# Kernel optimization log

Measured on AMD Instinct MI355X. Metric: run time of the kernel, lower is better.

The kernel has to match this reference:

```python
import jax, jax.numpy as jnp
import numpy as np

L, B, S, H = 13, 32, 128, 768   # encoder hidden states: layers, batch (hardcoded 32), seq, hidden
U = 32                          # num_gru_units
G = 2 * U                       # linear out dim / bidirectional GRU feature dim (64)
NL = 2                          # num_labels
EPS = 1e-3                      # keras LayerNormalization default epsilon


def setup_inputs() -> dict:
    key = jax.random.key(0)
    ks = jax.random.split(key, 10)
    def n(k, shape, scale=0.05):
        return (jax.random.normal(k, shape, jnp.float32) * scale).astype(jnp.float32)
    return {
        "xs": jax.random.normal(ks[0], (L, B, S, H), jnp.float32),
        "W_lin": n(ks[1], (H, G)),
        "b_lin": jnp.zeros((G,), jnp.float32),
        "ln_gamma": jnp.ones((G,), jnp.float32),
        "ln_beta": jnp.zeros((G,), jnp.float32),
        "Wk_f": n(ks[2], (G, 3 * U)),
        "Wr_f": n(ks[3], (U, 3 * U)),
        "b_f": jnp.zeros((2, 3 * U), jnp.float32),   # [input_bias, recurrent_bias] (reset_after=True)
        "Wk_b": n(ks[4], (G, 3 * U)),
        "Wr_b": n(ks[5], (U, 3 * U)),
        "b_b": jnp.zeros((2, 3 * U), jnp.float32),
        "W_cls": n(ks[6], (G, NL)),
        "b_cls": jnp.zeros((NL,), jnp.float32),
    }


def _layernorm(x, g, b):
    m = jnp.mean(x, axis=-1, keepdims=True)
    v = jnp.var(x, axis=-1, keepdims=True)
    return (x - m) * jax.lax.rsqrt(v + EPS) * g + b


def _gru_dir(seq, h0, Wk, Wr, bias):
    # Keras GRU v2 cell (reset_after=True). seq: [B,S,G], h0: [B,U]
    xp = jnp.einsum('bsg,gk->bsk', seq, Wk) + bias[0]  # [B,S,3U]
    def step(h, x_t):
        rec = h @ Wr + bias[1]                          # [B,3U]
        z = jax.nn.sigmoid(x_t[:, :U] + rec[:, :U])
        r = jax.nn.sigmoid(x_t[:, U:2 * U] + rec[:, U:2 * U])
        hh = jnp.tanh(x_t[:, 2 * U:] + r * rec[:, 2 * U:])
        hn = z * h + (1.0 - z) * hh
        return hn, hn
    hT, ys = jax.lax.scan(step, h0, jnp.swapaxes(xp, 0, 1))  # scan over time
    return jnp.swapaxes(ys, 0, 1), hT                        # [B,S,U], [B,U]


def reference(xs, W_lin, b_lin, ln_gamma, ln_beta,
              Wk_f, Wr_f, b_f, Wk_b, Wr_b, b_b, W_cls, b_cls):
    # _forward: loop over the 13 encoder hidden-state layers; the bidirectional
    # GRU output feeds back as a residual into the next layer's linear output.
    # Dropout layers are treated as identity (deterministic reference), under
    # which the 100-pass MC average equals a single pass.
    seq = jnp.zeros((B, S, G), xs.dtype)  # initial 'sequence' of zeros
    h1 = jnp.zeros((B, U), xs.dtype)      # initial_state=None -> zeros in keras
    h2 = jnp.zeros((B, U), xs.dtype)
    for i in range(L):
        x = _layernorm(xs[i] @ W_lin + b_lin + seq, ln_gamma, ln_beta)  # [B,S,G]
        out_f, h1 = _gru_dir(x, h1, Wk_f, Wr_f, b_f)
        out_b, h2 = _gru_dir(x[:, ::-1], h2, Wk_b, Wr_b, b_b)
        seq = jnp.concatenate([out_f, out_b[:, ::-1]], axis=-1)         # [B,S,2U]
    # tf.stack([h1,h2], -1) -> [B,U,2]; reshape [32,-1] interleaves fwd/bwd units
    hcat = jnp.stack([h1, h2], axis=-1).reshape(B, -1)                  # [B,2U]
    return jax.nn.softmax(hcat @ W_cls + b_cls, axis=-1)                # [B,NL]
```

## Files before the change

kernel.cpp:

```cpp
#include <hip/hip_runtime.h>
#include <hip/hip_fp16.h>

#define L_ 13
#define B_ 32
#define S_ 128
#define H_ 768
#define NU 32
#define GG 64
#define TU 96
#define LN_EPS 1e-3f
#define SEQ_ST 68
#define XT_ST 129
#define WK_ST 100
#define XPH_ST 100

#define DPP_X1  0xB1
#define DPP_X2  0x4E
#define DPP_X7  0x141
#define DPP_X15 0x140

typedef float v2f __attribute__((ext_vector_type(2)));
typedef _Float16 h2t __attribute__((ext_vector_type(2)));
typedef unsigned int uv2 __attribute__((ext_vector_type(2)));

union F4H8 { float4 f4; __half2 hh[4]; h2t h[4]; };
union FH2  { float f; __half2 hh; h2t h; };
union F2H2 { float2 f2; __half2 hh[2]; };

__device__ __forceinline__ float sigmoidf_(float a) { return 1.0f / (1.0f + __expf(-a)); }
__device__ __forceinline__ float tanhf_(float a) { float e = __expf(-2.0f * a); return (1.0f - e) / (1.0f + e); }
__device__ __forceinline__ void pkfma(v2f& a, v2f x, v2f w) {
    asm("v_pk_fma_f32 %0, %1, %2, %0" : "+v"(a) : "v"(x), "v"(w));
}
template <int CTRL>
__device__ __forceinline__ float dppf(float x) {
    return __int_as_float(__builtin_amdgcn_update_dpp(
        0, __float_as_int(x), CTRL, 0xF, 0xF, true));
}
__device__ __forceinline__ float pairsum16(float x) {
#if __has_builtin(__builtin_amdgcn_permlane16_swap)
    uv2 s = __builtin_amdgcn_permlane16_swap(
        __float_as_uint(x), __float_as_uint(x), false, false);
    return __uint_as_float(s.x) + __uint_as_float(s.y);
#else
    return x + __shfl_xor(x, 16);
#endif
}

__global__ __launch_bounds__(256) void lin_kernel(
    const float* __restrict__ xs, const float* __restrict__ Wl,
    const float* __restrict__ bl, __half* __restrict__ lin)
{
    __shared__ float sA[64][68];
    __shared__ float sW[64][68];
    const int t = threadIdx.x;
    const size_t row0 = (size_t)blockIdx.x * 64;
    const int r4 = (t >> 4) << 2;
    const int c4 = (t & 15) << 2;

    float acc[4][4];
    #pragma unroll
    for (int i = 0; i < 4; ++i)
        #pragma unroll
        for (int j = 0; j < 4; ++j) acc[i][j] = 0.f;

    for (int kt = 0; kt < H_; kt += 64) {
        #pragma unroll
        for (int p = 0; p < 4; ++p) {
            int idx = t + 256 * p;
            int r = idx >> 4, cc = (idx & 15) << 2;
            *(float4*)&sA[r][cc] = *(const float4*)&xs[(row0 + r) * H_ + kt + cc];
            *(float4*)&sW[r][cc] = *(const float4*)&Wl[(size_t)(kt + r) * GG + cc];
        }
        __syncthreads();
        #pragma unroll 8
        for (int k = 0; k < 64; ++k) {
            float a0 = sA[r4 + 0][k], a1 = sA[r4 + 1][k], a2 = sA[r4 + 2][k], a3 = sA[r4 + 3][k];
            float4 w = *(const float4*)&sW[k][c4];
            acc[0][0] += a0 * w.x; acc[0][1] += a0 * w.y; acc[0][2] += a0 * w.z; acc[0][3] += a0 * w.w;
            acc[1][0] += a1 * w.x; acc[1][1] += a1 * w.y; acc[1][2] += a1 * w.z; acc[1][3] += a1 * w.w;
            acc[2][0] += a2 * w.x; acc[2][1] += a2 * w.y; acc[2][2] += a2 * w.z; acc[2][3] += a2 * w.w;
            acc[3][0] += a3 * w.x; acc[3][1] += a3 * w.y; acc[3][2] += a3 * w.z; acc[3][3] += a3 * w.w;
        }
        __syncthreads();
    }
    float4 bv = *(const float4*)&bl[c4];
    #pragma unroll
    for (int i = 0; i < 4; ++i) {
        F2H2 u;
        u.hh[0] = __floats2half2_rn(acc[i][0] + bv.x, acc[i][1] + bv.y);
        u.hh[1] = __floats2half2_rn(acc[i][2] + bv.z, acc[i][3] + bv.w);
        *(float2*)&lin[(row0 + r4 + i) * GG + c4] = u.f2;
    }
}

__global__ __launch_bounds__(512) void chain_kernel(
    const __half* __restrict__ lin_all,
    const float* __restrict__ Wr_f, const float* __restrict__ b_f,
    const float* __restrict__ Wr_b, const float* __restrict__ b_b,
    const float* __restrict__ Wk_f, const float* __restrict__ Wk_b,
    const float* __restrict__ ln_g, const float* __restrict__ ln_b,
    const float* __restrict__ W_cls, const float* __restrict__ b_cls,
    float* __restrict__ out)
{
    extern __shared__ float sm[];
    float*   seqb = sm;
    __half2* xt2  = (__half2*)(sm + 8704);
    __half2* wk2  = (__half2*)(sm + 8704 + 4128);
    __half*  xph  = (__half*)(sm + 8704 + 4128 + 6400);
    float*   hbf  = sm + 8704 + 4128 + 6400 + 12800;
    float*   hbb  = hbf + NU;

    const int b = blockIdx.x;
    const int t = threadIdx.x;
    const int wave = t >> 6;
    const int lane = t & 63;
    const int v16 = lane & 15;
    const int b4 = (lane >> 4) & 1;
    const int b5 = (lane >> 5) & 1;
    const int ud = v16 + 16 * b5;

    for (int i = t; i < S_ * SEQ_ST; i += 512) seqb[i] = 0.f;
    for (int i = t; i < 2 * 32 * 96; i += 512) {
        const int d = i / 3072, rem = i - d * 3072, k2 = rem / 96, c = rem - k2 * 96;
        const float* W = d ? Wk_b : Wk_f;
        wk2[(d * 32 + k2) * WK_ST + c] =
            __floats2half2_rn(W[(2 * k2) * TU + c], W[(2 * k2 + 1) * TU + c]);
    }

    v2f wz[8], wr_[8], wh[8];
    float h_store = 0.f, h_dot = 0.f, rbz2 = 0.f, rbr2 = 0.f, rbh2 = 0.f;
    if (wave < 2) {
        const float* Wr   = wave ? Wr_b : Wr_f;
        const float* bias = wave ? b_b  : b_f;
        const int ex[8] = {0, 2, 7, 5, 15, 13, 8, 10};
        const int ey[8] = {1, 3, 6, 4, 14, 12, 9, 11};
        const int BB = 16 * b4;
        #pragma unroll
        for (int m = 0; m < 8; ++m) {
            const int jx = BB + (v16 ^ ex[m]), jy = BB + (v16 ^ ey[m]);
            wz[m]  = v2f{ Wr[jx * TU + ud],          Wr[jy * TU + ud] };
            wr_[m] = v2f{ Wr[jx * TU + NU + ud],     Wr[jy * TU + NU + ud] };
            wh[m]  = v2f{ Wr[jx * TU + 2 * NU + ud], Wr[jy * TU + 2 * NU + ud] };
        }
        rbz2 = 0.5f * bias[TU + ud];
        rbr2 = 0.5f * bias[TU + NU + ud];
        rbh2 = 0.5f * bias[TU + 2 * NU + ud];
    }

    const int g8 = t >> 3;
    const int c8 = (t & 7) << 3;
    const int rgrp = t & 31;
    const int cg = t >> 5;
    const int dsel = cg >> 3;
    const int cc = (cg & 7) * 12;
    const float* bias0 = dsel ? b_b : b_f;
    const __half2* wkd = wk2 + dsel * 32 * WK_ST;
    __half* xpd = xph + dsel * (S_ * XPH_ST);

    __syncthreads();

    for (int l = 0; l < L_; ++l) {
        const __half* linb = lin_all + (size_t)(l * B_ + b) * S_ * GG;

        #pragma unroll
        for (int p = 0; p < 2; ++p) {
            const int r = g8 + 64 * p;
            F4H8 lu; lu.f4 = *(const float4*)&linb[(size_t)r * GG + c8];
            float4 s0 = *(const float4*)&seqb[r * SEQ_ST + c8];
            float4 s1 = *(const float4*)&seqb[r * SEQ_ST + c8 + 4];
            float2 l0 = __half22float2(lu.hh[0]);
            float2 l1 = __half22float2(lu.hh[1]);
            float2 l2 = __half22float2(lu.hh[2]);
            float2 l3 = __half22float2(lu.hh[3]);
            float v[8];
            v[0] = l0.x + s0.x; v[1] = l0.y + s0.y; v[2] = l1.x + s0.z; v[3] = l1.y + s0.w;
            v[4] = l2.x + s1.x; v[5] = l2.y + s1.y; v[6] = l3.x + s1.z; v[7] = l3.y + s1.w;
            float s = 0.f;
            #pragma unroll
            for (int j = 0; j < 8; ++j) s += v[j];
            #pragma unroll
            for (int off = 1; off < 8; off <<= 1) s += __shfl_xor(s, off);
            const float mean = s * 0.015625f;
            float q = 0.f;
            float d[8];
            #pragma unroll
            for (int j = 0; j < 8; ++j) { d[j] = v[j] - mean; q += d[j] * d[j]; }
            #pragma unroll
            for (int off = 1; off < 8; off <<= 1) q += __shfl_xor(q, off);
            const float rstd = rsqrtf(q * 0.015625f + LN_EPS);
            float4 g0 = *(const float4*)&ln_g[c8];
            float4 g1 = *(const float4*)&ln_g[c8 + 4];
            float4 b0 = *(const float4*)&ln_b[c8];
            float4 b1 = *(const float4*)&ln_b[c8 + 4];
            float x[8];
            x[0] = d[0] * rstd * g0.x + b0.x; x[1] = d[1] * rstd * g0.y + b0.y;
            x[2] = d[2] * rstd * g0.z + b0.z; x[3] = d[3] * rstd * g0.w + b0.w;
            x[4] = d[4] * rstd * g1.x + b1.x; x[5] = d[5] * rstd * g1.y + b1.y;
            x[6] = d[6] * rstd * g1.z + b1.z; x[7] = d[7] * rstd * g1.w + b1.w;
            #pragma unroll
            for (int j = 0; j < 4; ++j)
                xt2[(c8 / 2 + j) * XT_ST + r] = __floats2half2_rn(x[2 * j], x[2 * j + 1]);
        }
        __syncthreads();

        {
            float acc[4][12];
            #pragma unroll
            for (int m = 0; m < 12; ++m) {
                const float bi = bias0[cc + m];
                acc[0][m] = bi; acc[1][m] = bi; acc[2][m] = bi; acc[3][m] = bi;
            }
            #pragma unroll 4
            for (int k2 = 0; k2 < 32; ++k2) {
                FH2 x0, x1, x2, x3;
                x0.hh = xt2[k2 * XT_ST + rgrp];
                x1.hh = xt2[k2 * XT_ST + rgrp + 32];
                x2.hh = xt2[k2 * XT_ST + rgrp + 64];
                x3.hh = xt2[k2 * XT_ST + rgrp + 96];
                F4H8 wa, wb, wc;
                wa.f4 = *(const float4*)&wkd[k2 * WK_ST + cc];
                wb.f4 = *(const float4*)&wkd[k2 * WK_ST + cc + 4];
                wc.f4 = *(const float4*)&wkd[k2 * WK_ST + cc + 8];
                #pragma unroll
                for (int m = 0; m < 4; ++m) {
                    acc[0][m]     = __builtin_amdgcn_fdot2(x0.h, wa.h[m], acc[0][m],     false);
                    acc[1][m]     = __builtin_amdgcn_fdot2(x1.h, wa.h[m], acc[1][m],     false);
                    acc[2][m]     = __builtin_amdgcn_fdot2(x2.h, wa.h[m], acc[2][m],     false);
                    acc[3][m]     = __builtin_amdgcn_fdot2(x3.h, wa.h[m], acc[3][m],     false);
                    acc[0][m + 4] = __builtin_amdgcn_fdot2(x0.h, wb.h[m], acc[0][m + 4], false);
                    acc[1][m + 4] = __builtin_amdgcn_fdot2(x1.h, wb.h[m], acc[1][m + 4], false);
                    acc[2][m + 4] = __builtin_amdgcn_fdot2(x2.h, wb.h[m], acc[2][m + 4], false);
                    acc[3][m + 4] = __builtin_amdgcn_fdot2(x3.h, wb.h[m], acc[3][m + 4], false);
                    acc[0][m + 8] = __builtin_amdgcn_fdot2(x0.h, wc.h[m], acc[0][m + 8], false);
                    acc[1][m + 8] = __builtin_amdgcn_fdot2(x1.h, wc.h[m], acc[1][m + 8], false);
                    acc[2][m + 8] = __builtin_amdgcn_fdot2(x2.h, wc.h[m], acc[2][m + 8], false);
                    acc[3][m + 8] = __builtin_amdgcn_fdot2(x3.h, wc.h[m], acc[3][m + 8], false);
                }
            }
            #pragma unroll
            for (int i = 0; i < 4; ++i) {
                const int r = rgrp + 32 * i;
                __half2* dst = (__half2*)&xpd[r * XPH_ST + cc];
                #pragma unroll
                for (int j = 0; j < 6; ++j)
                    dst[j] = __floats2half2_rn(acc[i][2 * j], acc[i][2 * j + 1]);
            }
        }
        __syncthreads();

        if (wave < 2) {
            const int dir = wave;
            const __half* xp = xph + dir * (S_ * XPH_ST);
            float* sq = seqb + dir * NU + (lane & 31);
            const int stp = dir ? -1 : 1;
            int s = dir ? (S_ - 1) : 0;
            const bool wl = (lane < 32);
            const bool fix = (b4 != b5);
            float xz = (float)xp[s * XPH_ST + ud];
            float xr = (float)xp[s * XPH_ST + 32 + ud];
            float xh = (float)xp[s * XPH_ST + 64 + ud];
            for (int st = 0; st < S_; ++st) {
                float nz = 0.f, nr = 0.f, nh = 0.f;
                if (st < S_ - 1) {
                    const int sn = s + stp;
                    nz = (float)xp[sn * XPH_ST + ud];
                    nr = (float)xp[sn * XPH_ST + 32 + ud];
                    nh = (float)xp[sn * XPH_ST + 64 + ud];
                }
                v2f ro[8];
                ro[0].x = h_store;                ro[0].y = dppf<DPP_X1>(h_store);
                ro[1].x = dppf<DPP_X2>(ro[0].x);  ro[1].y = dppf<DPP_X2>(ro[0].y);
                ro[2].x = dppf<DPP_X7>(ro[0].x);  ro[2].y = dppf<DPP_X7>(ro[0].y);
                ro[3].x = dppf<DPP_X7>(ro[1].x);  ro[3].y = dppf<DPP_X7>(ro[1].y);
                ro[4].x = dppf<DPP_X15>(ro[0].x); ro[4].y = dppf<DPP_X15>(ro[0].y);
                ro[5].x = dppf<DPP_X15>(ro[1].x); ro[5].y = dppf<DPP_X15>(ro[1].y);
                ro[6].x = dppf<DPP_X15>(ro[2].x); ro[6].y = dppf<DPP_X15>(ro[2].y);
                ro[7].x = dppf<DPP_X15>(ro[3].x); ro[7].y = dppf<DPP_X15>(ro[3].y);

                v2f az = v2f{0.5f * xz + rbz2, 0.f};
                v2f ar = v2f{0.5f * xr + rbr2, 0.f};
                v2f ah = v2f{rbh2, 0.f};
                #pragma unroll
                for (int m = 0; m < 8; ++m) {
                    pkfma(az, ro[m], wz[m]);
                    pkfma(ar, ro[m], wr_[m]);
                    pkfma(ah, ro[m], wh[m]);
                }
                const float pz = pairsum16(az.x + az.y);
                const float pr = pairsum16(ar.x + ar.y);
                const float ph = pairsum16(ah.x + ah.y);

                const float z  = sigmoidf_(pz);
                const float r  = sigmoidf_(pr);
                const float hh = tanhf_(xh + r * ph);
                const float hn_raw = hh + z * (h_dot - hh);
                h_dot = hn_raw;
                uv2 s32 = __builtin_amdgcn_permlane32_swap(
                    __float_as_uint(hn_raw), __float_as_uint(hn_raw), false, false);
                const float v32 = wl ? __uint_as_float(s32.y) : __uint_as_float(s32.x);
                h_store = fix ? v32 : hn_raw;
                if (wl) sq[s * SEQ_ST] = h_store;
                s += stp; xz = nz; xr = nr; xh = nh;
            }
        }
        __syncthreads();
    }

    if (wave < 2 && lane < 32) (wave ? hbb : hbf)[lane & 31] = h_store;
    __syncthreads();
    if (t == 0) {
        float l0 = b_cls[0], l1 = b_cls[1];
        for (int j = 0; j < NU; ++j) {
            const float hf = hbf[j], hk = hbb[j];
            l0 += hf * W_cls[4 * j]     + hk * W_cls[4 * j + 2];
            l1 += hf * W_cls[4 * j + 1] + hk * W_cls[4 * j + 3];
        }
        const float m = fmaxf(l0, l1);
        const float e0 = __expf(l0 - m), e1 = __expf(l1 - m);
        const float inv = 1.0f / (e0 + e1);
        out[b * 2 + 0] = e0 * inv;
        out[b * 2 + 1] = e1 * inv;
    }
}

extern "C" void kernel_launch(void* const* d_in, const int* in_sizes, int n_in,
                              void* d_out, int out_size, void* d_ws, size_t ws_size,
                              hipStream_t stream) {
    const float* xs    = (const float*)d_in[0];
    const float* W_lin = (const float*)d_in[1];
    const float* b_lin = (const float*)d_in[2];
    const float* ln_g  = (const float*)d_in[3];
    const float* ln_b  = (const float*)d_in[4];
    const float* Wk_f  = (const float*)d_in[5];
    const float* Wr_f  = (const float*)d_in[6];
    const float* b_f   = (const float*)d_in[7];
    const float* Wk_b  = (const float*)d_in[8];
    const float* Wr_b  = (const float*)d_in[9];
    const float* b_b   = (const float*)d_in[10];
    const float* W_cls = (const float*)d_in[11];
    const float* b_cls = (const float*)d_in[12];
    float* out = (float*)d_out;

    __half* lin_all = (__half*)d_ws;

    const int smem = (8704 + 4128 + 6400 + 12800 + 64) * (int)sizeof(float);
    (void)hipFuncSetAttribute((const void*)chain_kernel,
                              hipFuncAttributeMaxDynamicSharedMemorySize, smem);

    lin_kernel<<<(L_ * B_ * S_) / 64, 256, 0, stream>>>(xs, W_lin, b_lin, lin_all);

    chain_kernel<<<B_, 512, smem, stream>>>(
        lin_all, Wr_f, b_f, Wr_b, b_b, Wk_f, Wk_b, ln_g, ln_b, W_cls, b_cls, out);
}
```

Measured before the change: 639.8 us.

## Overlap per-layer LayerNorm and input projection with GRU recurrence via LDS flags

Replaces the block-wide barrier sequence (LN, projection GEMM, recurrence) with producer/consumer specialization inside the block. Six waves compute LN and the input projection in row chunks ordered from the sequence centre outward. They publish completion counters in LDS, and the two recurrence waves poll those counters before consuming each chunk. The recurrence waves likewise publish progress so the next layer's chunks can start as soon as their inputs are ready. Separately, the activations now use exp2 and rcp with log2e prescaling folded into the weights and biases, and the accumulation chains are split in two to shorten dependencies. The spin-waits with sleep add polling overhead and carry some ordering risk.

```diff
diff --git a/kernel.cpp b/kernel.cpp
--- a/kernel.cpp
+++ b/kernel.cpp
@@ -10,15 +10,23 @@
 #define TU 96
 #define LN_EPS 1e-3f
 #define SEQ_ST 68
-#define XT_ST 129
 #define WK_ST 100
 #define XPH_ST 100
+#define K1f 1.4426950408889634f
+#define K2f 2.8853900817779268f
 
 #define DPP_X1  0xB1
 #define DPP_X2  0x4E
 #define DPP_X7  0x141
 #define DPP_X15 0x140
 
+#define OFF_WK   8704
+#define OFF_XPH  (OFF_WK + 6400)
+#define OFF_XT2  (OFF_XPH + 12800)
+#define OFF_HB   (OFF_XT2 + 3456)
+#define OFF_FLG  (OFF_HB + 64)
+#define SMEM_FLOATS (OFF_FLG + 32)
+
 typedef float v2f __attribute__((ext_vector_type(2)));
 typedef _Float16 h2t __attribute__((ext_vector_type(2)));
 typedef unsigned int uv2 __attribute__((ext_vector_type(2)));
@@ -27,8 +35,6 @@
 union FH2  { float f; __half2 hh; h2t h; };
 union F2H2 { float2 f2; __half2 hh[2]; };
 
-__device__ __forceinline__ float sigmoidf_(float a) { return 1.0f / (1.0f + __expf(-a)); }
-__device__ __forceinline__ float tanhf_(float a) { float e = __expf(-2.0f * a); return (1.0f - e) / (1.0f + e); }
 __device__ __forceinline__ void pkfma(v2f& a, v2f x, v2f w) {
     asm("v_pk_fma_f32 %0, %1, %2, %0" : "+v"(a) : "v"(x), "v"(w));
 }
@@ -45,6 +51,16 @@
 #else
     return x + __shfl_xor(x, 16);
 #endif
+}
+__device__ __forceinline__ int chunk_of(int r) {
+    return (r < 64) ? ((63 - r) >> 3) : ((r - 64) >> 3);
+}
+__device__ __forceinline__ void poll_ge(unsigned* p, unsigned tgt) {
+    int gd = 0;
+    while (__hip_atomic_load(p, __ATOMIC_ACQUIRE, __HIP_MEMORY_SCOPE_WORKGROUP) < tgt) {
+        __builtin_amdgcn_s_sleep(1);
+        if (++gd > (1 << 24)) break;
+    }
 }
 
 __global__ __launch_bounds__(256) void lin_kernel(
@@ -104,12 +120,14 @@
     float* __restrict__ out)
 {
     extern __shared__ float sm[];
-    float*   seqb = sm;
-    __half2* xt2  = (__half2*)(sm + 8704);
-    __half2* wk2  = (__half2*)(sm + 8704 + 4128);
-    __half*  xph  = (__half*)(sm + 8704 + 4128 + 6400);
-    float*   hbf  = sm + 8704 + 4128 + 6400 + 12800;
-    float*   hbb  = hbf + NU;
+    float*    seqb   = sm;
+    __half2*  wk2    = (__half2*)(sm + OFF_WK);
+    __half*   xph    = (__half*)(sm + OFF_XPH);
+    __half2*  xt2all = (__half2*)(sm + OFF_XT2);
+    float*    hbf    = sm + OFF_HB;
+    float*    hbb    = hbf + NU;
+    unsigned* seq_blk = (unsigned*)(sm + OFF_FLG);
+    unsigned* gemcnt  = seq_blk + 16;
 
     const int b = blockIdx.x;
     const int t = threadIdx.x;
@@ -121,11 +139,13 @@
     const int ud = v16 + 16 * b5;
 
     for (int i = t; i < S_ * SEQ_ST; i += 512) seqb[i] = 0.f;
+    if (t < 24) seq_blk[t] = 0u;
     for (int i = t; i < 2 * 32 * 96; i += 512) {
         const int d = i / 3072, rem = i - d * 3072, k2 = rem / 96, c = rem - k2 * 96;
         const float* W = d ? Wk_b : Wk_f;
+        const float sc = (c >= 64) ? K2f : K1f;
         wk2[(d * 32 + k2) * WK_ST + c] =
-            __floats2half2_rn(W[(2 * k2) * TU + c], W[(2 * k2 + 1) * TU + c]);
+            __floats2half2_rn(W[(2 * k2) * TU + c] * sc, W[(2 * k2 + 1) * TU + c] * sc);
     }
 
     v2f wz[8], wr_[8], wh[8];
@@ -139,134 +159,45 @@
         #pragma unroll
         for (int m = 0; m < 8; ++m) {
             const int jx = BB + (v16 ^ ex[m]), jy = BB + (v16 ^ ey[m]);
-            wz[m]  = v2f{ Wr[jx * TU + ud],          Wr[jy * TU + ud] };
-            wr_[m] = v2f{ Wr[jx * TU + NU + ud],     Wr[jy * TU + NU + ud] };
-            wh[m]  = v2f{ Wr[jx * TU + 2 * NU + ud], Wr[jy * TU + 2 * NU + ud] };
-        }
-        rbz2 = 0.5f * bias[TU + ud];
-        rbr2 = 0.5f * bias[TU + NU + ud];
-        rbh2 = 0.5f * bias[TU + 2 * NU + ud];
-    }
-
-    const int g8 = t >> 3;
-    const int c8 = (t & 7) << 3;
-    const int rgrp = t & 31;
-    const int cg = t >> 5;
-    const int dsel = cg >> 3;
-    const int cc = (cg & 7) * 12;
-    const float* bias0 = dsel ? b_b : b_f;
-    const __half2* wkd = wk2 + dsel * 32 * WK_ST;
-    __half* xpd = xph + dsel * (S_ * XPH_ST);
+            wz[m]  = v2f{ K1f * Wr[jx * TU + ud],          K1f * Wr[jy * TU + ud] };
+            wr_[m] = v2f{ K1f * Wr[jx * TU + NU + ud],     K1f * Wr[jy * TU + NU + ud] };
+            wh[m]  = v2f{ K2f * Wr[jx * TU + 2 * NU + ud], K2f * Wr[jy * TU + 2 * NU + ud] };
+        }
+        rbz2 = 0.5f * K1f * bias[TU + ud];
+        rbr2 = 0.5f * K1f * bias[TU + NU + ud];
+        rbh2 = 0.5f * K2f * bias[TU + 2 * NU + ud];
+    }
 
     __syncthreads();
 
-    for (int l = 0; l < L_; ++l) {
-        const __half* linb = lin_all + (size_t)(l * B_ + b) * S_ * GG;
-
-        #pragma unroll
-        for (int p = 0; p < 2; ++p) {
-            const int r = g8 + 64 * p;
-            F4H8 lu; lu.f4 = *(const float4*)&linb[(size_t)r * GG + c8];
-            float4 s0 = *(const float4*)&seqb[r * SEQ_ST + c8];
-            float4 s1 = *(const float4*)&seqb[r * SEQ_ST + c8 + 4];
-            float2 l0 = __half22float2(lu.hh[0]);
-            float2 l1 = __half22float2(lu.hh[1]);
-            float2 l2 = __half22float2(lu.hh[2]);
-            float2 l3 = __half22float2(lu.hh[3]);
-            float v[8];
-            v[0] = l0.x + s0.x; v[1] = l0.y + s0.y; v[2] = l1.x + s0.z; v[3] = l1.y + s0.w;
-            v[4] = l2.x + s1.x; v[5] = l2.y + s1.y; v[6] = l3.x + s1.z; v[7] = l3.y + s1.w;
-            float s = 0.f;
-            #pragma unroll
-            for (int j = 0; j < 8; ++j) s += v[j];
-            #pragma unroll
-            for (int off = 1; off < 8; off <<= 1) s += __shfl_xor(s, off);
-            const float mean = s * 0.015625f;
-            float q = 0.f;
-            float d[8];
-            #pragma unroll
-            for (int j = 0; j < 8; ++j) { d[j] = v[j] - mean; q += d[j] * d[j]; }
-            #pragma unroll
-            for (int off = 1; off < 8; off <<= 1) q += __shfl_xor(q, off);
-            const float rstd = rsqrtf(q * 0.015625f + LN_EPS);
-            float4 g0 = *(const float4*)&ln_g[c8];
-            float4 g1 = *(const float4*)&ln_g[c8 + 4];
-            float4 b0 = *(const float4*)&ln_b[c8];
-            float4 b1 = *(const float4*)&ln_b[c8 + 4];
-            float x[8];
-            x[0] = d[0] * rstd * g0.x + b0.x; x[1] = d[1] * rstd * g0.y + b0.y;
-            x[2] = d[2] * rstd * g0.z + b0.z; x[3] = d[3] * rstd * g0.w + b0.w;
-            x[4] = d[4] * rstd * g1.x + b1.x; x[5] = d[5] * rstd * g1.y + b1.y;
-            x[6] = d[6] * rstd * g1.z + b1.z; x[7] = d[7] * rstd * g1.w + b1.w;
-            #pragma unroll
-            for (int j = 0; j < 4; ++j)
-                xt2[(c8 / 2 + j) * XT_ST + r] = __floats2half2_rn(x[2 * j], x[2 * j + 1]);
-        }
-        __syncthreads();
-
-        {
-            float acc[4][12];
-            #pragma unroll
-            for (int m = 0; m < 12; ++m) {
-                const float bi = bias0[cc + m];
-                acc[0][m] = bi; acc[1][m] = bi; acc[2][m] = bi; acc[3][m] = bi;
-            }
-            #pragma unroll 4
-            for (int k2 = 0; k2 < 32; ++k2) {
-                FH2 x0, x1, x2, x3;
-                x0.hh = xt2[k2 * XT_ST + rgrp];
-                x1.hh = xt2[k2 * XT_ST + rgrp + 32];
-                x2.hh = xt2[k2 * XT_ST + rgrp + 64];
-                x3.hh = xt2[k2 * XT_ST + rgrp + 96];
-                F4H8 wa, wb, wc;
-                wa.f4 = *(const float4*)&wkd[k2 * WK_ST + cc];
-                wb.f4 = *(const float4*)&wkd[k2 * WK_ST + cc + 4];
-                wc.f4 = *(const float4*)&wkd[k2 * WK_ST + cc + 8];
-                #pragma unroll
-                for (int m = 0; m < 4; ++m) {
-                    acc[0][m]     = __builtin_amdgcn_fdot2(x0.h, wa.h[m], acc[0][m],     false);
-                    acc[1][m]     = __builtin_amdgcn_fdot2(x1.h, wa.h[m], acc[1][m],     false);
-                    acc[2][m]     = __builtin_amdgcn_fdot2(x2.h, wa.h[m], acc[2][m],     false);
-                    acc[3][m]     = __builtin_amdgcn_fdot2(x3.h, wa.h[m], acc[3][m],     false);
-                    acc[0][m + 4] = __builtin_amdgcn_fdot2(x0.h, wb.h[m], acc[0][m + 4], false);
-                    acc[1][m + 4] = __builtin_amdgcn_fdot2(x1.h, wb.h[m], acc[1][m + 4], false);
-                    acc[2][m + 4] = __builtin_amdgcn_fdot2(x2.h, wb.h[m], acc[2][m + 4], false);
-                    acc[3][m + 4] = __builtin_amdgcn_fdot2(x3.h, wb.h[m], acc[3][m + 4], false);
-                    acc[0][m + 8] = __builtin_amdgcn_fdot2(x0.h, wc.h[m], acc[0][m + 8], false);
-                    acc[1][m + 8] = __builtin_amdgcn_fdot2(x1.h, wc.h[m], acc[1][m + 8], false);
-                    acc[2][m + 8] = __builtin_amdgcn_fdot2(x2.h, wc.h[m], acc[2][m + 8], false);
-                    acc[3][m + 8] = __builtin_amdgcn_fdot2(x3.h, wc.h[m], acc[3][m + 8], false);
-                }
-            }
-            #pragma unroll
-            for (int i = 0; i < 4; ++i) {
-                const int r = rgrp + 32 * i;
-                __half2* dst = (__half2*)&xpd[r * XPH_ST + cc];
-                #pragma unroll
-                for (int j = 0; j < 6; ++j)
-                    dst[j] = __floats2half2_rn(acc[i][2 * j], acc[i][2 * j + 1]);
-            }
-        }
-        __syncthreads();
-
-        if (wave < 2) {
-            const int dir = wave;
-            const __half* xp = xph + dir * (S_ * XPH_ST);
-            float* sq = seqb + dir * NU + (lane & 31);
-            const int stp = dir ? -1 : 1;
+    if (wave < 2) {
+        const int dir = wave;
+        const __half* xp = xph + dir * (S_ * XPH_ST);
+        float* sq = seqb + dir * NU + (lane & 31);
+        const int stp = dir ? -1 : 1;
+        const bool wl = (lane < 32);
+        const bool fix = (b4 != b5);
+
+        for (int L = 0; L < L_; ++L) {
+            unsigned dmask = 0;
+            poll_ge(&gemcnt[7], (unsigned)(L + 1));
+            dmask |= 1u << 7;
             int s = dir ? (S_ - 1) : 0;
-            const bool wl = (lane < 32);
-            const bool fix = (b4 != b5);
             float xz = (float)xp[s * XPH_ST + ud];
             float xr = (float)xp[s * XPH_ST + 32 + ud];
             float xh = (float)xp[s * XPH_ST + 64 + ud];
             for (int st = 0; st < S_; ++st) {
                 float nz = 0.f, nr = 0.f, nh = 0.f;
                 if (st < S_ - 1) {
-                    const int sn = s + stp;
-                    nz = (float)xp[sn * XPH_ST + ud];
-                    nr = (float)xp[sn * XPH_ST + 32 + ud];
-                    nh = (float)xp[sn * XPH_ST + 64 + ud];
+                    const int rp = s + stp;
+                    const int g = chunk_of(rp);
+                    if (!((dmask >> g) & 1u)) {
+                        poll_ge(&gemcnt[g], (unsigned)(L + 1));
+                        dmask |= 1u << g;
+                    }
+                    nz = (float)xp[rp * XPH_ST + ud];
+                    nr = (float)xp[rp * XPH_ST + 32 + ud];
+                    nh = (float)xp[rp * XPH_ST + 64 + ud];
                 }
                 v2f ro[8];
                 ro[0].x = h_store;                ro[0].y = dppf<DPP_X1>(h_store);
@@ -278,22 +209,25 @@
                 ro[6].x = dppf<DPP_X15>(ro[2].x); ro[6].y = dppf<DPP_X15>(ro[2].y);
                 ro[7].x = dppf<DPP_X15>(ro[3].x); ro[7].y = dppf<DPP_X15>(ro[3].y);
 
-                v2f az = v2f{0.5f * xz + rbz2, 0.f};
-                v2f ar = v2f{0.5f * xr + rbr2, 0.f};
-                v2f ah = v2f{rbh2, 0.f};
+                v2f aza = v2f{0.5f * xz + rbz2, 0.f}, azb = v2f{0.f, 0.f};
+                v2f ara = v2f{0.5f * xr + rbr2, 0.f}, arb = v2f{0.f, 0.f};
+                v2f aha = v2f{rbh2, 0.f},             ahb = v2f{0.f, 0.f};
                 #pragma unroll
-                for (int m = 0; m < 8; ++m) {
-                    pkfma(az, ro[m], wz[m]);
-                    pkfma(ar, ro[m], wr_[m]);
-                    pkfma(ah, ro[m], wh[m]);
-                }
-                const float pz = pairsum16(az.x + az.y);
-                const float pr = pairsum16(ar.x + ar.y);
-                const float ph = pairsum16(ah.x + ah.y);
-
-                const float z  = sigmoidf_(pz);
-                const float r  = sigmoidf_(pr);
-                const float hh = tanhf_(xh + r * ph);
+                for (int m = 0; m < 4; ++m) {
+                    pkfma(aza, ro[m], wz[m]);      pkfma(azb, ro[m + 4], wz[m + 4]);
+                    pkfma(ara, ro[m], wr_[m]);     pkfma(arb, ro[m + 4], wr_[m + 4]);
+                    pkfma(aha, ro[m], wh[m]);      pkfma(ahb, ro[m + 4], wh[m + 4]);
+                }
+                v2f azs = aza + azb, ars = ara + arb, ahs = aha + ahb;
+                const float pz = pairsum16(azs.x + azs.y);
+                const float pr = pairsum16(ars.x + ars.y);
+                const float ph = pairsum16(ahs.x + ahs.y);
+
+                const float z  = __builtin_amdgcn_rcpf(1.0f + __builtin_amdgcn_exp2f(-pz));
+                const float r  = __builtin_amdgcn_rcpf(1.0f + __builtin_amdgcn_exp2f(-pr));
+                const float tt = xh + r * ph;
+                const float et = __builtin_amdgcn_exp2f(-tt);
+                const float hh = (1.0f - et) * __builtin_amdgcn_rcpf(1.0f + et);
                 const float hn_raw = hh + z * (h_dot - hh);
                 h_dot = hn_raw;
                 uv2 s32 = __builtin_amdgcn_permlane32_swap(
@@ -301,13 +235,120 @@
                 const float v32 = wl ? __uint_as_float(s32.y) : __uint_as_float(s32.x);
                 h_store = fix ? v32 : hn_raw;
                 if (wl) sq[s * SEQ_ST] = h_store;
+                const bool pub = dir ? ((s & 15) == 0) : ((s & 15) == 15);
+                if (pub && lane == 0)
+                    __hip_atomic_store(&seq_blk[dir * 8 + (s >> 4)], (unsigned)(L + 1),
+                                       __ATOMIC_RELEASE, __HIP_MEMORY_SCOPE_WORKGROUP);
                 s += stp; xz = nz; xr = nr; xh = nh;
             }
         }
-        __syncthreads();
-    }
-
-    if (wave < 2 && lane < 32) (wave ? hbb : hbf)[lane & 31] = h_store;
+        if (wl) (dir ? hbb : hbf)[lane & 31] = h_store;
+    } else {
+        const int w = wave - 2;
+        __half2* xt2w = xt2all + w * 576;
+        const int c4 = (lane & 15) << 2;
+        const int g16 = lane >> 4;
+        const int lr4 = lane & 3;
+        const int cg = lane >> 2;
+        const int dsel = cg >> 3;
+        const int cc = (cg & 7) * 12;
+        const float* bias0 = dsel ? b_b : b_f;
+        const __half2* wkd = wk2 + dsel * 32 * WK_ST;
+        __half* xpd = xph + dsel * (S_ * XPH_ST);
+        float bsc[12];
+        #pragma unroll
+        for (int m = 0; m < 12; ++m)
+            bsc[m] = bias0[cc + m] * ((cc + m >= 64) ? K2f : K1f);
+
+        for (int L = 0; L < L_; ++L) {
+            const __half* linb = lin_all + (size_t)(L * B_ + b) * S_ * GG;
+            #pragma unroll 1
+            for (int g = 0; g < 8; ++g) {
+                if ((L * 8 + g) % 6 != w) continue;
+                const int bl = (56 - 8 * g) >> 4;
+                const int rA = 56 - 8 * g, rB = 64 + 8 * g;
+                poll_ge(&seq_blk[bl], (unsigned)L);
+                poll_ge(&seq_blk[7 - bl], (unsigned)L);
+                poll_ge(&seq_blk[8 + bl], (unsigned)L);
+                poll_ge(&seq_blk[8 + 7 - bl], (unsigned)L);
+
+                #pragma unroll
+                for (int p = 0; p < 4; ++p) {
+                    const int lr = 4 * p + g16;
+                    const int r = (lr < 8) ? (rA + lr) : (rB + lr - 8);
+                    F2H2 lu; lu.f2 = *(const float2*)&linb[(size_t)r * GG + c4];
+                    float4 sv = *(const float4*)&seqb[r * SEQ_ST + c4];
+                    float2 l0 = __half22float2(lu.hh[0]);
+                    float2 l1 = __half22float2(lu.hh[1]);
+                    float v0 = l0.x + sv.x, v1 = l0.y + sv.y, v2 = l1.x + sv.z, v3 = l1.y + sv.w;
+                    float s = v0 + v1 + v2 + v3;
+                    #pragma unroll
+                    for (int off = 1; off < 16; off <<= 1) s += __shfl_xor(s, off);
+                    const float mean = s * 0.015625f;
+                    const float d0 = v0 - mean, d1 = v1 - mean, d2 = v2 - mean, d3 = v3 - mean;
+                    float q = d0 * d0 + d1 * d1 + d2 * d2 + d3 * d3;
+                    #pragma unroll
+                    for (int off = 1; off < 16; off <<= 1) q += __shfl_xor(q, off);
+                    const float rstd = rsqrtf(q * 0.015625f + LN_EPS);
+                    float4 gm = *(const float4*)&ln_g[c4];
+                    float4 bt = *(const float4*)&ln_b[c4];
+                    const float x0 = d0 * rstd * gm.x + bt.x;
+                    const float x1 = d1 * rstd * gm.y + bt.y;
+                    const float x2 = d2 * rstd * gm.z + bt.z;
+                    const float x3 = d3 * rstd * gm.w + bt.w;
+                    const int k2a = (lane & 15) << 1;
+                    xt2w[(k2a + 0) * 18 + lr] = __floats2half2_rn(x0, x1);
+                    xt2w[(k2a + 1) * 18 + lr] = __floats2half2_rn(x2, x3);
+                }
+
+                float acc[4][12];
+                #pragma unroll
+                for (int m = 0; m < 12; ++m) {
+                    acc[0][m] = bsc[m]; acc[1][m] = bsc[m]; acc[2][m] = bsc[m]; acc[3][m] = bsc[m];
+                }
+                #pragma unroll 4
+                for (int k2 = 0; k2 < 32; ++k2) {
+                    FH2 x0, x1, x2, x3;
+                    x0.hh = xt2w[k2 * 18 + lr4];
+                    x1.hh = xt2w[k2 * 18 + lr4 + 4];
+                    x2.hh = xt2w[k2 * 18 + lr4 + 8];
+                    x3.hh = xt2w[k2 * 18 + lr4 + 12];
+                    F4H8 wa, wb, wc;
+                    wa.f4 = *(const float4*)&wkd[k2 * WK_ST + cc];
+                    wb.f4 = *(const float4*)&wkd[k2 * WK_ST + cc + 4];
+                    wc.f4 = *(const float4*)&wkd[k2 * WK_ST + cc + 8];
+                    #pragma unroll
+                    for (int m = 0; m < 4; ++m) {
+                        acc[0][m]     = __builtin_amdgcn_fdot2(x0.h, wa.h[m], acc[0][m],     false);
+                        acc[1][m]     = __builtin_amdgcn_fdot2(x1.h, wa.h[m], acc[1][m],     false);
+                        acc[2][m]     = __builtin_amdgcn_fdot2(x2.h, wa.h[m], acc[2][m],     false);
+                        acc[3][m]     = __builtin_amdgcn_fdot2(x3.h, wa.h[m], acc[3][m],     false);
+                        acc[0][m + 4] = __builtin_amdgcn_fdot2(x0.h, wb.h[m], acc[0][m + 4], false);
+                        acc[1][m + 4] = __builtin_amdgcn_fdot2(x1.h, wb.h[m], acc[1][m + 4], false);
+                        acc[2][m + 4] = __builtin_amdgcn_fdot2(x2.h, wb.h[m], acc[2][m + 4], false);
+                        acc[3][m + 4] = __builtin_amdgcn_fdot2(x3.h, wb.h[m], acc[3][m + 4], false);
+                        acc[0][m + 8] = __builtin_amdgcn_fdot2(x0.h, wc.h[m], acc[0][m + 8], false);
+                        acc[1][m + 8] = __builtin_amdgcn_fdot2(x1.h, wc.h[m], acc[1][m + 8], false);
+                        acc[2][m + 8] = __builtin_amdgcn_fdot2(x2.h, wc.h[m], acc[2][m + 8], false);
+                        acc[3][m + 8] = __builtin_amdgcn_fdot2(x3.h, wc.h[m], acc[3][m + 8], false);
+                    }
+                }
+                #pragma unroll
+                for (int i = 0; i < 4; ++i) {
+                    const int lr = lr4 + 4 * i;
+                    const int r = (lr < 8) ? (rA + lr) : (rB + lr - 8);
+                    __half2* dst = (__half2*)&xpd[r * XPH_ST + cc];
+                    #pragma unroll
+                    for (int j = 0; j < 6; ++j)
+                        dst[j] = __floats2half2_rn(acc[i][2 * j], acc[i][2 * j + 1]);
+                }
+                if (lane == 0)
+                    __hip_atomic_store(&gemcnt[g], (unsigned)(L + 1),
+                                       __ATOMIC_RELEASE, __HIP_MEMORY_SCOPE_WORKGROUP);
+            }
+        }
+    }
+
     __syncthreads();
     if (t == 0) {
         float l0 = b_cls[0], l1 = b_cls[1];
@@ -344,7 +385,7 @@
 
     __half* lin_all = (__half*)d_ws;
 
-    const int smem = (8704 + 4128 + 6400 + 12800 + 64) * (int)sizeof(float);
+    const int smem = SMEM_FLOATS * (int)sizeof(float);
     (void)hipFuncSetAttribute((const void*)chain_kernel,
                               hipFuncAttributeMaxDynamicSharedMemorySize, smem);
 
```

After: 752.9 us. 1.18x slower.

## Run both GRU directions interleaved in one wave with exp2-prescaled gates

Applied to the files above, without the earlier changes.

Puts the forward and backward GRU recurrences into a single wavefront that interleaves the two independent chains, giving each instruction stream twice the ILP to hide DPP, permlane and transcendental latency. Input and recurrent weights and biases are prescaled by log2(e) (or 2·log2(e) for the candidate gate), so sigmoid and tanh use raw exp2 and rcp intrinsics. The FMA chains are also split into two partial accumulators to shorten dependency depth. The cost is higher register pressure in wave 0 and serial issue of two directions' work on one SIMD instead of two waves.

```diff
diff --git a/kernel.cpp b/kernel.cpp
--- a/kernel.cpp
+++ b/kernel.cpp
@@ -13,6 +13,8 @@
 #define XT_ST 129
 #define WK_ST 100
 #define XPH_ST 100
+#define K1f 1.4426950408889634f
+#define K2f 2.8853900817779268f
 
 #define DPP_X1  0xB1
 #define DPP_X2  0x4E
@@ -27,8 +29,6 @@
 union FH2  { float f; __half2 hh; h2t h; };
 union F2H2 { float2 f2; __half2 hh[2]; };
 
-__device__ __forceinline__ float sigmoidf_(float a) { return 1.0f / (1.0f + __expf(-a)); }
-__device__ __forceinline__ float tanhf_(float a) { float e = __expf(-2.0f * a); return (1.0f - e) / (1.0f + e); }
 __device__ __forceinline__ void pkfma(v2f& a, v2f x, v2f w) {
     asm("v_pk_fma_f32 %0, %1, %2, %0" : "+v"(a) : "v"(x), "v"(w));
 }
@@ -45,6 +45,16 @@
 #else
     return x + __shfl_xor(x, 16);
 #endif
+}
+__device__ __forceinline__ void butterfly(float h, v2f ro[8]) {
+    ro[0].x = h;                      ro[0].y = dppf<DPP_X1>(h);
+    ro[1].x = dppf<DPP_X2>(ro[0].x);  ro[1].y = dppf<DPP_X2>(ro[0].y);
+    ro[2].x = dppf<DPP_X7>(ro[0].x);  ro[2].y = dppf<DPP_X7>(ro[0].y);
+    ro[3].x = dppf<DPP_X7>(ro[1].x);  ro[3].y = dppf<DPP_X7>(ro[1].y);
+    ro[4].x = dppf<DPP_X15>(ro[0].x); ro[4].y = dppf<DPP_X15>(ro[0].y);
+    ro[5].x = dppf<DPP_X15>(ro[1].x); ro[5].y = dppf<DPP_X15>(ro[1].y);
+    ro[6].x = dppf<DPP_X15>(ro[2].x); ro[6].y = dppf<DPP_X15>(ro[2].y);
+    ro[7].x = dppf<DPP_X15>(ro[3].x); ro[7].y = dppf<DPP_X15>(ro[3].y);
 }
 
 __global__ __launch_bounds__(256) void lin_kernel(
@@ -124,28 +134,34 @@
     for (int i = t; i < 2 * 32 * 96; i += 512) {
         const int d = i / 3072, rem = i - d * 3072, k2 = rem / 96, c = rem - k2 * 96;
         const float* W = d ? Wk_b : Wk_f;
+        const float sc = (c >= 64) ? K2f : K1f;
         wk2[(d * 32 + k2) * WK_ST + c] =
-            __floats2half2_rn(W[(2 * k2) * TU + c], W[(2 * k2 + 1) * TU + c]);
-    }
-
-    v2f wz[8], wr_[8], wh[8];
-    float h_store = 0.f, h_dot = 0.f, rbz2 = 0.f, rbr2 = 0.f, rbh2 = 0.f;
-    if (wave < 2) {
-        const float* Wr   = wave ? Wr_b : Wr_f;
-        const float* bias = wave ? b_b  : b_f;
+            __floats2half2_rn(W[(2 * k2) * TU + c] * sc, W[(2 * k2 + 1) * TU + c] * sc);
+    }
+
+    v2f wzf[8], wrf[8], whf[8], wzb[8], wrb[8], whb[8];
+    float hsf = 0.f, hdf = 0.f, hsb = 0.f, hdb = 0.f;
+    float rbzf = 0.f, rbrf = 0.f, rbhf = 0.f, rbzb = 0.f, rbrb = 0.f, rbhb = 0.f;
+    if (wave == 0) {
         const int ex[8] = {0, 2, 7, 5, 15, 13, 8, 10};
         const int ey[8] = {1, 3, 6, 4, 14, 12, 9, 11};
         const int BB = 16 * b4;
         #pragma unroll
         for (int m = 0; m < 8; ++m) {
             const int jx = BB + (v16 ^ ex[m]), jy = BB + (v16 ^ ey[m]);
-            wz[m]  = v2f{ Wr[jx * TU + ud],          Wr[jy * TU + ud] };
-            wr_[m] = v2f{ Wr[jx * TU + NU + ud],     Wr[jy * TU + NU + ud] };
-            wh[m]  = v2f{ Wr[jx * TU + 2 * NU + ud], Wr[jy * TU + 2 * NU + ud] };
-        }
-        rbz2 = 0.5f * bias[TU + ud];
-        rbr2 = 0.5f * bias[TU + NU + ud];
-        rbh2 = 0.5f * bias[TU + 2 * NU + ud];
+            wzf[m] = v2f{ K1f * Wr_f[jx * TU + ud],          K1f * Wr_f[jy * TU + ud] };
+            wrf[m] = v2f{ K1f * Wr_f[jx * TU + NU + ud],     K1f * Wr_f[jy * TU + NU + ud] };
+            whf[m] = v2f{ K2f * Wr_f[jx * TU + 2 * NU + ud], K2f * Wr_f[jy * TU + 2 * NU + ud] };
+            wzb[m] = v2f{ K1f * Wr_b[jx * TU + ud],          K1f * Wr_b[jy * TU + ud] };
+            wrb[m] = v2f{ K1f * Wr_b[jx * TU + NU + ud],     K1f * Wr_b[jy * TU + NU + ud] };
+            whb[m] = v2f{ K2f * Wr_b[jx * TU + 2 * NU + ud], K2f * Wr_b[jy * TU + 2 * NU + ud] };
+        }
+        rbzf = 0.5f * K1f * b_f[TU + ud];
+        rbrf = 0.5f * K1f * b_f[TU + NU + ud];
+        rbhf = 0.5f * K2f * b_f[TU + 2 * NU + ud];
+        rbzb = 0.5f * K1f * b_b[TU + ud];
+        rbrb = 0.5f * K1f * b_b[TU + NU + ud];
+        rbhb = 0.5f * K2f * b_b[TU + 2 * NU + ud];
     }
 
     const int g8 = t >> 3;
@@ -157,6 +173,10 @@
     const float* bias0 = dsel ? b_b : b_f;
     const __half2* wkd = wk2 + dsel * 32 * WK_ST;
     __half* xpd = xph + dsel * (S_ * XPH_ST);
+    float bsc[12];
+    #pragma unroll
+    for (int m = 0; m < 12; ++m)
+        bsc[m] = bias0[cc + m] * ((cc + m >= 64) ? K2f : K1f);
 
     __syncthreads();
 
@@ -208,8 +228,7 @@
             float acc[4][12];
             #pragma unroll
             for (int m = 0; m < 12; ++m) {
-                const float bi = bias0[cc + m];
-                acc[0][m] = bi; acc[1][m] = bi; acc[2][m] = bi; acc[3][m] = bi;
+                acc[0][m] = bsc[m]; acc[1][m] = bsc[m]; acc[2][m] = bsc[m]; acc[3][m] = bsc[m];
             }
             #pragma unroll 4
             for (int k2 = 0; k2 < 32; ++k2) {
@@ -249,65 +268,98 @@
         }
         __syncthreads();
 
-        if (wave < 2) {
-            const int dir = wave;
-            const __half* xp = xph + dir * (S_ * XPH_ST);
-            float* sq = seqb + dir * NU + (lane & 31);
-            const int stp = dir ? -1 : 1;
-            int s = dir ? (S_ - 1) : 0;
+        if (wave == 0) {
+            const __half* xf = xph;
+            const __half* xb = xph + S_ * XPH_ST;
+            float* sqf = seqb + (lane & 31);
+            float* sqb_ = seqb + NU + (lane & 31);
             const bool wl = (lane < 32);
             const bool fix = (b4 != b5);
-            float xz = (float)xp[s * XPH_ST + ud];
-            float xr = (float)xp[s * XPH_ST + 32 + ud];
-            float xh = (float)xp[s * XPH_ST + 64 + ud];
+            int sf = 0, sb = S_ - 1;
+            float xzf = (float)xf[sf * XPH_ST + ud];
+            float xrf = (float)xf[sf * XPH_ST + 32 + ud];
+            float xhf = (float)xf[sf * XPH_ST + 64 + ud];
+            float xzb = (float)xb[sb * XPH_ST + ud];
+            float xrb = (float)xb[sb * XPH_ST + 32 + ud];
+            float xhb = (float)xb[sb * XPH_ST + 64 + ud];
             for (int st = 0; st < S_; ++st) {
-                float nz = 0.f, nr = 0.f, nh = 0.f;
+                float nzf = 0.f, nrf = 0.f, nhf = 0.f, nzb = 0.f, nrb = 0.f, nhb = 0.f;
                 if (st < S_ - 1) {
-                    const int sn = s + stp;
-                    nz = (float)xp[sn * XPH_ST + ud];
-                    nr = (float)xp[sn * XPH_ST + 32 + ud];
-                    nh = (float)xp[sn * XPH_ST + 64 + ud];
+                    nzf = (float)xf[(sf + 1) * XPH_ST + ud];
+                    nrf = (float)xf[(sf + 1) * XPH_ST + 32 + ud];
+                    nhf = (float)xf[(sf + 1) * XPH_ST + 64 + ud];
+                    nzb = (float)xb[(sb - 1) * XPH_ST + ud];
+                    nrb = (float)xb[(sb - 1) * XPH_ST + 32 + ud];
+                    nhb = (float)xb[(sb - 1) * XPH_ST + 64 + ud];
                 }
-                v2f ro[8];
-                ro[0].x = h_store;                ro[0].y = dppf<DPP_X1>(h_store);
-                ro[1].x = dppf<DPP_X2>(ro[0].x);  ro[1].y = dppf<DPP_X2>(ro[0].y);
-                ro[2].x = dppf<DPP_X7>(ro[0].x);  ro[2].y = dppf<DPP_X7>(ro[0].y);
-                ro[3].x = dppf<DPP_X7>(ro[1].x);  ro[3].y = dppf<DPP_X7>(ro[1].y);
-                ro[4].x = dppf<DPP_X15>(ro[0].x); ro[4].y = dppf<DPP_X15>(ro[0].y);
-                ro[5].x = dppf<DPP_X15>(ro[1].x); ro[5].y = dppf<DPP_X15>(ro[1].y);
-                ro[6].x = dppf<DPP_X15>(ro[2].x); ro[6].y = dppf<DPP_X15>(ro[2].y);
-                ro[7].x = dppf<DPP_X15>(ro[3].x); ro[7].y = dppf<DPP_X15>(ro[3].y);
-
-                v2f az = v2f{0.5f * xz + rbz2, 0.f};
-                v2f ar = v2f{0.5f * xr + rbr2, 0.f};
-                v2f ah = v2f{rbh2, 0.f};
+                v2f rof[8], rob[8];
+                butterfly(hsf, rof);
+                butterfly(hsb, rob);
+
+                v2f azf = v2f{0.5f * xzf + rbzf, 0.f};
+                v2f arf = v2f{0.5f * xrf + rbrf, 0.f};
+                v2f ahf = v2f{rbhf, 0.f};
+                v2f azb = v2f{0.5f * xzb + rbzb, 0.f};
+                v2f arb = v2f{0.5f * xrb + rbrb, 0.f};
+                v2f ahb = v2f{rbhb, 0.f};
+                v2f azf2 = v2f{0.f, 0.f}, arf2 = v2f{0.f, 0.f}, ahf2 = v2f{0.f, 0.f};
+                v2f azb2 = v2f{0.f, 0.f}, arb2 = v2f{0.f, 0.f}, ahb2 = v2f{0.f, 0.f};
                 #pragma unroll
-                for (int m = 0; m < 8; ++m) {
-                    pkfma(az, ro[m], wz[m]);
-                    pkfma(ar, ro[m], wr_[m]);
-                    pkfma(ah, ro[m], wh[m]);
+                for (int m = 0; m < 4; ++m) {
+                    pkfma(azf, rof[m], wzf[m]);      pkfma(azf2, rof[m + 4], wzf[m + 4]);
+                    pkfma(azb, rob[m], wzb[m]);      pkfma(azb2, rob[m + 4], wzb[m + 4]);
+                    pkfma(arf, rof[m], wrf[m]);      pkfma(arf2, rof[m + 4], wrf[m + 4]);
+                    pkfma(arb, rob[m], wrb[m]);      pkfma(arb2, rob[m + 4], wrb[m + 4]);
+                    pkfma(ahf, rof[m], whf[m]);      pkfma(ahf2, rof[m + 4], whf[m + 4]);
+                    pkfma(ahb, rob[m], whb[m]);      pkfma(ahb2, rob[m + 4], whb[m + 4]);
                 }
-                const float pz = pairsum16(az.x + az.y);
-                const float pr = pairsum16(ar.x + ar.y);
-                const float ph = pairsum16(ah.x + ah.y);
-
-                const float z  = sigmoidf_(pz);
-                const float r  = sigmoidf_(pr);
-                const float hh = tanhf_(xh + r * ph);
-                const float hn_raw = hh + z * (h_dot - hh);
-                h_dot = hn_raw;
-                uv2 s32 = __builtin_amdgcn_permlane32_swap(
-                    __float_as_uint(hn_raw), __float_as_uint(hn_raw), false, false);
-                const float v32 = wl ? __uint_as_float(s32.y) : __uint_as_float(s32.x);
-                h_store = fix ? v32 : hn_raw;
-                if (wl) sq[s * SEQ_ST] = h_store;
-                s += stp; xz = nz; xr = nr; xh = nh;
+                v2f azfs = azf + azf2, arfs = arf + arf2, ahfs = ahf + ahf2;
+                v2f azbs = azb + azb2, arbs = arb + arb2, ahbs = ahb + ahb2;
+                const float pzf = pairsum16(azfs.x + azfs.y);
+                const float pzb = pairsum16(azbs.x + azbs.y);
+                const float prf = pairsum16(arfs.x + arfs.y);
+                const float prb = pairsum16(arbs.x + arbs.y);
+                const float phf = pairsum16(ahfs.x + ahfs.y);
+                const float phb = pairsum16(ahbs.x + ahbs.y);
+
+                const float zf = __builtin_amdgcn_rcpf(1.0f + __builtin_amdgcn_exp2f(-pzf));
+                const float zb = __builtin_amdgcn_rcpf(1.0f + __builtin_amdgcn_exp2f(-pzb));
+                const float rf = __builtin_amdgcn_rcpf(1.0f + __builtin_amdgcn_exp2f(-prf));
+                const float rb = __builtin_amdgcn_rcpf(1.0f + __builtin_amdgcn_exp2f(-prb));
+                const float ttf = xhf + rf * phf;
+                const float ttb = xhb + rb * phb;
+                const float etf = __builtin_amdgcn_exp2f(-ttf);
+                const float etb = __builtin_amdgcn_exp2f(-ttb);
+                const float hhf = (1.0f - etf) * __builtin_amdgcn_rcpf(1.0f + etf);
+                const float hhb = (1.0f - etb) * __builtin_amdgcn_rcpf(1.0f + etb);
+                const float hnf = hhf + zf * (hdf - hhf);
+                const float hnb = hhb + zb * (hdb - hhb);
+                hdf = hnf; hdb = hnb;
+
+                uv2 swf = __builtin_amdgcn_permlane32_swap(
+                    __float_as_uint(hnf), __float_as_uint(hnf), false, false);
+                uv2 swb = __builtin_amdgcn_permlane32_swap(
+                    __float_as_uint(hnb), __float_as_uint(hnb), false, false);
+                const float vf = wl ? __uint_as_float(swf.y) : __uint_as_float(swf.x);
+                const float vb = wl ? __uint_as_float(swb.y) : __uint_as_float(swb.x);
+                hsf = fix ? vf : hnf;
+                hsb = fix ? vb : hnb;
+                if (wl) {
+                    sqf[sf * SEQ_ST] = hsf;
+                    sqb_[sb * SEQ_ST] = hsb;
+                }
+                ++sf; --sb;
+                xzf = nzf; xrf = nrf; xhf = nhf;
+                xzb = nzb; xrb = nrb; xhb = nhb;
             }
         }
         __syncthreads();
     }
 
-    if (wave < 2 && lane < 32) (wave ? hbb : hbf)[lane & 31] = h_store;
+    if (wave == 0 && lane < 32) {
+        hbf[lane & 31] = hsf;
+        hbb[lane & 31] = hsb;
+    }
     __syncthreads();
     if (t == 0) {
         float l0 = b_cls[0], l1 = b_cls[1];
```

Result: slower. 907.6 us (+41.9%).
